# Kernel optimization log

Measured on AMD Instinct MI355X. Metric: run time of the kernel, lower is better.

## Reference

```python
import jax, jax.numpy as jnp
import numpy as np

B, S, H, E = 2, 2048, 16, 64
INV_SCALE = 8.0  # sqrt(head_dim); forward divides scores by this


def setup_inputs() -> dict:
    key = jax.random.key(0)
    ks = jax.random.split(key, 10)
    return {
        "query": jax.random.normal(ks[0], (B, S, H, E), dtype=jnp.float32),
        "key": jax.random.normal(ks[1], (B, S, H, E), dtype=jnp.float32),
        "value": jax.random.normal(ks[2], (B, S, H, E), dtype=jnp.float32),
        "attn_mask": jax.random.randint(ks[3], (B, S), 0, 2, dtype=jnp.int32),
        "Wq": jax.random.normal(ks[4], (E, E), dtype=jnp.float32) / np.sqrt(E),
        "bq": jax.random.normal(ks[5], (E,), dtype=jnp.float32) * 0.02,
        "Wk": jax.random.normal(ks[6], (E, E), dtype=jnp.float32) / np.sqrt(E),
        "bk": jax.random.normal(ks[7], (E,), dtype=jnp.float32) * 0.02,
        "Wv": jax.random.normal(ks[8], (E, E), dtype=jnp.float32) / np.sqrt(E),
        "bv": jax.random.normal(ks[9], (E,), dtype=jnp.float32) * 0.02,
    }


def reference(query, key, value, attn_mask, Wq, bq, Wk, bk, Wv, bv):
    # Linear projections over the last (embed) dim; torch Linear: x @ W.T + b
    q = jnp.einsum('bshe,fe->bhsf', query, Wq) + bq  # [B,H,S,E] (permute 0,2,1,3 fused)
    k = jnp.einsum('bshe,fe->bhsf', key, Wk) + bk
    v = jnp.einsum('bshe,fe->bhsf', value, Wv) + bv
    scores = jnp.einsum('bhqe,bhke->bhqk', q, k) / INV_SCALE  # [B,H,S,S]
    # mask: positions where attn_mask == 0 get -inf, broadcast over (1,1,k_len)
    masked = attn_mask[:, None, None, :] == 0  # [B,1,1,S]
    scores = jnp.where(masked, -jnp.inf, scores)
    attn = jax.nn.softmax(scores, axis=-1)
    out = jnp.einsum('bhqk,bhke->bqhe', attn, v)  # permute back to [B,S,H,E]
    return out
```

## Files before the change

kernel.cpp:

```cpp
#include <hip/hip_runtime.h>


#define BATCH 2
#define SEQ   2048
#define NH    16
#define DE    64
#define LDP   72
#define LDOF  68
#define NKT   (SEQ / 64)
#define LOG2E 1.44269504088896340736f
#define CSHIFT 16.0f

using bf16x8   = __attribute__((ext_vector_type(8))) __bf16;
using bf16x4   = __attribute__((ext_vector_type(4))) __bf16;
using floatx4  = __attribute__((ext_vector_type(4))) float;
using ushortx4 = __attribute__((ext_vector_type(4))) unsigned short;
using ushortx8 = __attribute__((ext_vector_type(8))) unsigned short;

__device__ __forceinline__ ushortx4 cvt4(floatx4 f) {
    bf16x4 h = __builtin_convertvector(f, bf16x4);
    return __builtin_bit_cast(ushortx4, h);
}

__device__ __forceinline__ void glds16(const unsigned short* g, unsigned short* l) {
    __builtin_amdgcn_global_load_lds(
        (const __attribute__((address_space(1))) unsigned int*)g,
        (__attribute__((address_space(3))) unsigned int*)l, 16, 0, 0);
}

__global__ __launch_bounds__(256) void proj_kernel(
    const float* __restrict__ xq, const float* __restrict__ xk, const float* __restrict__ xv,
    const float* __restrict__ Wq, const float* __restrict__ bq,
    const float* __restrict__ Wk, const float* __restrict__ bk,
    const float* __restrict__ Wv, const float* __restrict__ bv,
    unsigned short* __restrict__ qb, unsigned short* __restrict__ kb,
    unsigned short* __restrict__ vtb)
{
    __shared__ __align__(16) unsigned short Xb[64 * LDP];
    __shared__ __align__(16) unsigned short Wb[64 * LDP];
    __shared__ __align__(16) unsigned short Ob[64 * LDP];
    __shared__ float blds[64];

    const int t  = threadIdx.x;
    const int p  = blockIdx.x >> 10;
    const int bh = (blockIdx.x >> 5) & 31;
    const int st = blockIdx.x & 31;
    const int s0 = st * 64;
    const int b  = bh >> 4, h = bh & 15;
    const int lane = t & 63, w = t >> 6, quad = lane >> 4, l16 = lane & 15;

    const float* x    = (p == 0) ? xq : (p == 1) ? xk : xv;
    const float* W    = (p == 0) ? Wq : (p == 1) ? Wk : Wv;
    const float* bias = (p == 0) ? bq : (p == 1) ? bk : bv;

    #pragma unroll
    for (int i = 0; i < 4; ++i) {
        int idx = i * 1024 + t * 4;
        int row = idx >> 6, col = idx & 63;
        floatx4 xv4 = *(const floatx4*)(x + (((size_t)(b * SEQ + s0 + row) * NH + h) * DE + col));
        *(ushortx4*)&Xb[row * LDP + col] = cvt4(xv4);
        floatx4 wv4 = *(const floatx4*)(W + row * 64 + col);
        *(ushortx4*)&Wb[row * LDP + col] = cvt4(wv4);
    }
    if (t < 64) blds[t] = bias[t];
    __syncthreads();

    if (p < 2) {
        bf16x8 a0 = *(const bf16x8*)&Wb[(w * 16 + l16) * LDP + quad * 8];
        bf16x8 a1 = *(const bf16x8*)&Wb[(w * 16 + l16) * LDP + 32 + quad * 8];
        floatx4 bf4 = *(const floatx4*)&blds[w * 16 + quad * 4];
        const float scale = (p == 0) ? 0.125f * LOG2E : 1.0f;
        #pragma unroll
        for (int nb = 0; nb < 4; ++nb) {
            bf16x8 b0 = *(const bf16x8*)&Xb[(nb * 16 + l16) * LDP + quad * 8];
            bf16x8 b1 = *(const bf16x8*)&Xb[(nb * 16 + l16) * LDP + 32 + quad * 8];
            floatx4 c = {0.f, 0.f, 0.f, 0.f};
            c = __builtin_amdgcn_mfma_f32_16x16x32_bf16(a0, b0, c, 0, 0, 0);
            c = __builtin_amdgcn_mfma_f32_16x16x32_bf16(a1, b1, c, 0, 0, 0);
            floatx4 v;
            v[0] = (c[0] + bf4[0]) * scale; v[1] = (c[1] + bf4[1]) * scale;
            v[2] = (c[2] + bf4[2]) * scale; v[3] = (c[3] + bf4[3]) * scale;
            *(ushortx4*)&Ob[(nb * 16 + l16) * LDP + w * 16 + quad * 4] = cvt4(v);
        }
    } else {
        bf16x8 a0 = *(const bf16x8*)&Xb[(w * 16 + l16) * LDP + quad * 8];
        bf16x8 a1 = *(const bf16x8*)&Xb[(w * 16 + l16) * LDP + 32 + quad * 8];
        #pragma unroll
        for (int nb = 0; nb < 4; ++nb) {
            bf16x8 b0 = *(const bf16x8*)&Wb[(nb * 16 + l16) * LDP + quad * 8];
            bf16x8 b1 = *(const bf16x8*)&Wb[(nb * 16 + l16) * LDP + 32 + quad * 8];
            floatx4 c = {0.f, 0.f, 0.f, 0.f};
            c = __builtin_amdgcn_mfma_f32_16x16x32_bf16(a0, b0, c, 0, 0, 0);
            c = __builtin_amdgcn_mfma_f32_16x16x32_bf16(a1, b1, c, 0, 0, 0);
            float bw = blds[nb * 16 + l16];
            floatx4 v;
            v[0] = c[0] + bw; v[1] = c[1] + bw; v[2] = c[2] + bw; v[3] = c[3] + bw;
            *(ushortx4*)&Ob[(nb * 16 + l16) * LDP + w * 16 + quad * 4] = cvt4(v);
        }
    }
    __syncthreads();

    #pragma unroll
    for (int j = 0; j < 2; ++j) {
        int idx = j * 256 + t;
        int row = idx >> 3, c = idx & 7;
        int cp  = (c ^ (row & 7)) * 8;
        ushortx8 v = *(const ushortx8*)&Ob[row * LDP + c * 8];
        if (p < 2) {
            unsigned short* dst = (p == 0) ? qb : kb;
            *(ushortx8*)(dst + ((size_t)bh * SEQ + s0 + row) * DE + cp) = v;
        } else {
            *(ushortx8*)(vtb + ((size_t)bh * DE + row) * SEQ + s0 + cp) = v;
        }
    }
}

__global__ __launch_bounds__(512) void attn_kernel(
    const unsigned short* __restrict__ qb, const unsigned short* __restrict__ kb,
    const unsigned short* __restrict__ vtb, const int* __restrict__ mask,
    float* __restrict__ out)
{
    __shared__ __align__(16) char smem[16384 + 16384 + 18432 + 512];
    unsigned short* Kl = (unsigned short*)smem;
    unsigned short* Vl = (unsigned short*)(smem + 16384);
    unsigned short* Pq = (unsigned short*)(smem + 32768);
    float*          Ml = (float*)(smem + 32768 + 18432);
    float*          Ol = (float*)smem;

    const int t  = threadIdx.x;
    const int qt = blockIdx.x, bh = blockIdx.y;
    const int b  = bh >> 4, h = bh & 15;
    const int q0 = qt * 128;
    const int lane = t & 63, w = t >> 6;
    const int quad = lane >> 4, l16 = lane & 15;
    const int cS = ((quad ^ (l16 & 7)) * 8);

    const unsigned short* kbase = kb + (size_t)bh * SEQ * DE;
    const unsigned short* vbase = vtb + (size_t)bh * DE * SEQ;
    const unsigned short* qsrc  = qb + ((size_t)bh * SEQ + q0) * DE;
    const int* mrow = mask + b * SEQ;

    glds16(qsrc + (w * 16) * DE + lane * 8,      Pq + (w * 16) * 64);
    glds16(qsrc + (w * 16 + 8) * DE + lane * 8,  Pq + (w * 16 + 8) * 64);
    glds16(kbase + (size_t)(w * 8) * DE + lane * 8, Kl + w * 512);
    glds16(vbase + (size_t)(w * 8 + (lane >> 3)) * SEQ + (lane & 7) * 8, Vl + w * 512);
    if (t < 64) Ml[t] = mrow[t] ? 0.f : -1e30f;
    int mreg = (t < 64) ? mrow[64 + t] : 0;
    __syncthreads();

    bf16x8 qf0 = *(const bf16x8*)&Pq[(w * 16 + l16) * 64 + cS];
    bf16x8 qf1 = *(const bf16x8*)&Pq[(w * 16 + l16) * 64 + (cS ^ 32)];

    bf16x8 onesf;
    #pragma unroll
    for (int i = 0; i < 8; ++i) onesf[i] = (__bf16)1.0f;

    floatx4 o[4], acc_l;
    #pragma unroll
    for (int nb = 0; nb < 4; ++nb) o[nb] = floatx4{0.f, 0.f, 0.f, 0.f};
    acc_l = floatx4{0.f, 0.f, 0.f, 0.f};

    for (int kt = 0; kt < NKT; ++kt) {
        const int cur = kt & 1, nxt = cur ^ 1;
        const unsigned short* Kc = Kl + cur * 4096;
        const unsigned short* Vc = Vl + cur * 4096;
        const float*          Mc = Ml + cur * 64;

        if (kt + 1 < NKT) {
            const int k1 = (kt + 1) * 64;
            glds16(kbase + (size_t)(k1 + w * 8) * DE + lane * 8, Kl + nxt * 4096 + w * 512);
            glds16(vbase + (size_t)(w * 8 + (lane >> 3)) * SEQ + k1 + (lane & 7) * 8,
                   Vl + nxt * 4096 + w * 512);
            if (t < 64) Ml[nxt * 64 + t] = mreg ? 0.f : -1e30f;
            mreg = (t < 64 && kt + 2 < NKT) ? mrow[(kt + 2) * 64 + t] : 0;
        }

        floatx4 sc[4];
        #pragma unroll
        for (int sub = 0; sub < 4; ++sub) {
            const int r = sub * 16 + l16;
            bf16x8 kf0 = *(const bf16x8*)&Kc[r * 64 + cS];
            bf16x8 kf1 = *(const bf16x8*)&Kc[r * 64 + (cS ^ 32)];
            floatx4 c = *(const floatx4*)&Mc[sub * 16 + quad * 4];
            c = __builtin_amdgcn_mfma_f32_16x16x32_bf16(kf0, qf0, c, 0, 0, 0);
            c = __builtin_amdgcn_mfma_f32_16x16x32_bf16(kf1, qf1, c, 0, 0, 0);
            sc[sub] = c;
        }

        #pragma unroll
        for (int sub = 0; sub < 4; ++sub) {
            #pragma unroll
            for (int r = 0; r < 4; ++r)
                sc[sub][r] = __builtin_amdgcn_exp2f(sc[sub][r] - CSHIFT);
            *(ushortx4*)&Pq[(w * 16 + l16) * LDP + sub * 16 + quad * 4] = cvt4(sc[sub]);
        }
        __asm__ volatile("s_waitcnt lgkmcnt(0)" ::: "memory");

        bf16x8 pf0 = *(const bf16x8*)&Pq[(w * 16 + l16) * LDP + quad * 8];
        bf16x8 pf1 = *(const bf16x8*)&Pq[(w * 16 + l16) * LDP + 32 + quad * 8];
        #pragma unroll
        for (int nb = 0; nb < 4; ++nb) {
            const int r = nb * 16 + l16;
            bf16x8 vf0 = *(const bf16x8*)&Vc[r * 64 + cS];
            bf16x8 vf1 = *(const bf16x8*)&Vc[r * 64 + (cS ^ 32)];
            o[nb] = __builtin_amdgcn_mfma_f32_16x16x32_bf16(vf0, pf0, o[nb], 0, 0, 0);
            o[nb] = __builtin_amdgcn_mfma_f32_16x16x32_bf16(vf1, pf1, o[nb], 0, 0, 0);
        }
        acc_l = __builtin_amdgcn_mfma_f32_16x16x32_bf16(onesf, pf0, acc_l, 0, 0, 0);
        acc_l = __builtin_amdgcn_mfma_f32_16x16x32_bf16(onesf, pf1, acc_l, 0, 0, 0);

        __syncthreads();
    }

    float invl = __builtin_amdgcn_rcpf(acc_l[0]);
    #pragma unroll
    for (int nb = 0; nb < 4; ++nb) {
        floatx4 ov;
        ov[0] = o[nb][0] * invl; ov[1] = o[nb][1] * invl;
        ov[2] = o[nb][2] * invl; ov[3] = o[nb][3] * invl;
        *(floatx4*)&Ol[(w * 16 + l16) * LDOF + nb * 16 + quad * 4] = ov;
    }
    __asm__ volatile("s_waitcnt lgkmcnt(0)" ::: "memory");
    #pragma unroll
    for (int pass = 0; pass < 4; ++pass) {
        int rl  = w * 16 + pass * 4 + quad;
        int col = l16 * 4;
        floatx4 tv = *(const floatx4*)&Ol[rl * LDOF + col];
        *(floatx4*)(out + (((size_t)b * SEQ + q0 + rl) * NH + h) * DE + col) = tv;
    }
}

extern "C" void kernel_launch(void* const* d_in, const int* in_sizes, int n_in,
                              void* d_out, int out_size, void* d_ws, size_t ws_size,
                              hipStream_t stream) {
    const float* query = (const float*)d_in[0];
    const float* key   = (const float*)d_in[1];
    const float* value = (const float*)d_in[2];
    const int*   mask  = (const int*)d_in[3];
    const float* Wq = (const float*)d_in[4];
    const float* bq = (const float*)d_in[5];
    const float* Wk = (const float*)d_in[6];
    const float* bk = (const float*)d_in[7];
    const float* Wv = (const float*)d_in[8];
    const float* bv = (const float*)d_in[9];

    const size_t tensor_elems = (size_t)BATCH * NH * SEQ * DE;
    unsigned short* qb  = (unsigned short*)d_ws;
    unsigned short* kb  = qb + tensor_elems;
    unsigned short* vtb = kb + tensor_elems;

    proj_kernel<<<dim3(3 * BATCH * NH * (SEQ / 64)), 256, 0, stream>>>(
        query, key, value, Wq, bq, Wk, bk, Wv, bv, qb, kb, vtb);
    attn_kernel<<<dim3(SEQ / 128, BATCH * NH), 512, 0, stream>>>(
        qb, kb, vtb, mask, (float*)d_out);
}
```

Baseline: 158.5 us.

## Switch attention to 32x32x16 MFMA with in-register P via permlane32 swap

Restructures the attention inner loop to use 32x32x16 bf16 MFMAs. Each wave now owns 32 query rows and half of the 64-key block, and the per-tile split results are combined through LDS at the end. The softmax probabilities are packed to bf16 and rearranged in registers with v_permlane32_swap instead of a round trip through LDS. The row sum is accumulated with scalar adds rather than extra ones-MFMAs, and the exp shift is folded into the mask bias. In exchange it adds a cross-wave reduction epilogue with extra syncs, and sets launch bounds to request 4 blocks per SM.

```diff
diff --git a/kernel.cpp b/kernel.cpp
--- a/kernel.cpp
+++ b/kernel.cpp
@@ -13,13 +13,26 @@
 
 using bf16x8   = __attribute__((ext_vector_type(8))) __bf16;
 using bf16x4   = __attribute__((ext_vector_type(4))) __bf16;
+using bf16x2   = __attribute__((ext_vector_type(2))) __bf16;
+using floatx2  = __attribute__((ext_vector_type(2))) float;
 using floatx4  = __attribute__((ext_vector_type(4))) float;
+using floatx16 = __attribute__((ext_vector_type(16))) float;
 using ushortx4 = __attribute__((ext_vector_type(4))) unsigned short;
 using ushortx8 = __attribute__((ext_vector_type(8))) unsigned short;
+using uintx4   = __attribute__((ext_vector_type(4))) unsigned int;
 
 __device__ __forceinline__ ushortx4 cvt4(floatx4 f) {
     bf16x4 h = __builtin_convertvector(f, bf16x4);
     return __builtin_bit_cast(ushortx4, h);
+}
+
+__device__ __forceinline__ unsigned int pkbf16(float a, float b) {
+    floatx2 f = {a, b};
+    return __builtin_bit_cast(unsigned int, __builtin_convertvector(f, bf16x2));
+}
+
+__device__ __forceinline__ void pl32swap(unsigned int& x, unsigned int& y) {
+    __asm__ volatile("v_permlane32_swap_b32 %0, %1" : "+v"(x), "+v"(y));
 }
 
 __device__ __forceinline__ void glds16(const unsigned short* g, unsigned short* l) {
@@ -115,25 +128,27 @@
     }
 }
 
-__global__ __launch_bounds__(512) void attn_kernel(
+__global__ __launch_bounds__(512, 4) void attn_kernel(
     const unsigned short* __restrict__ qb, const unsigned short* __restrict__ kb,
     const unsigned short* __restrict__ vtb, const int* __restrict__ mask,
     float* __restrict__ out)
 {
-    __shared__ __align__(16) char smem[16384 + 16384 + 18432 + 512];
+    __shared__ __align__(16) char smem[16384 + 16384 + 16384 + 512];
     unsigned short* Kl = (unsigned short*)smem;
     unsigned short* Vl = (unsigned short*)(smem + 16384);
     unsigned short* Pq = (unsigned short*)(smem + 32768);
-    float*          Ml = (float*)(smem + 32768 + 18432);
+    float*          Ml = (float*)(smem + 49152);
     float*          Ol = (float*)smem;
+    float*          Ll = (float*)(smem + 34816);
 
     const int t  = threadIdx.x;
     const int qt = blockIdx.x, bh = blockIdx.y;
     const int b  = bh >> 4, h = bh & 15;
     const int q0 = qt * 128;
     const int lane = t & 63, w = t >> 6;
-    const int quad = lane >> 4, l16 = lane & 15;
-    const int cS = ((quad ^ (l16 & 7)) * 8);
+    const int hi = lane >> 5, l31 = lane & 31;
+    const int qw = w & 3, kblk = w >> 2;
+    const int sw7 = l31 & 7;
 
     const unsigned short* kbase = kb + (size_t)bh * SEQ * DE;
     const unsigned short* vbase = vtb + (size_t)bh * DE * SEQ;
@@ -144,21 +159,19 @@
     glds16(qsrc + (w * 16 + 8) * DE + lane * 8,  Pq + (w * 16 + 8) * 64);
     glds16(kbase + (size_t)(w * 8) * DE + lane * 8, Kl + w * 512);
     glds16(vbase + (size_t)(w * 8 + (lane >> 3)) * SEQ + (lane & 7) * 8, Vl + w * 512);
-    if (t < 64) Ml[t] = mrow[t] ? 0.f : -1e30f;
+    if (t < 64) Ml[t] = mrow[t] ? -CSHIFT : -1e30f;
     int mreg = (t < 64) ? mrow[64 + t] : 0;
     __syncthreads();
 
-    bf16x8 qf0 = *(const bf16x8*)&Pq[(w * 16 + l16) * 64 + cS];
-    bf16x8 qf1 = *(const bf16x8*)&Pq[(w * 16 + l16) * 64 + (cS ^ 32)];
-
-    bf16x8 onesf;
+    bf16x8 qf[4];
     #pragma unroll
-    for (int i = 0; i < 8; ++i) onesf[i] = (__bf16)1.0f;
-
-    floatx4 o[4], acc_l;
+    for (int ks = 0; ks < 4; ++ks)
+        qf[ks] = *(const bf16x8*)&Pq[(qw * 32 + l31) * 64 + (((ks * 2 + hi) ^ sw7) * 8)];
+
+    floatx16 o0, o1;
     #pragma unroll
-    for (int nb = 0; nb < 4; ++nb) o[nb] = floatx4{0.f, 0.f, 0.f, 0.f};
-    acc_l = floatx4{0.f, 0.f, 0.f, 0.f};
+    for (int i = 0; i < 16; ++i) { o0[i] = 0.f; o1[i] = 0.f; }
+    float lp = 0.f;
 
     for (int kt = 0; kt < NKT; ++kt) {
         const int cur = kt & 1, nxt = cur ^ 1;
@@ -171,62 +184,95 @@
             glds16(kbase + (size_t)(k1 + w * 8) * DE + lane * 8, Kl + nxt * 4096 + w * 512);
             glds16(vbase + (size_t)(w * 8 + (lane >> 3)) * SEQ + k1 + (lane & 7) * 8,
                    Vl + nxt * 4096 + w * 512);
-            if (t < 64) Ml[nxt * 64 + t] = mreg ? 0.f : -1e30f;
+            if (t < 64) Ml[nxt * 64 + t] = mreg ? -CSHIFT : -1e30f;
             mreg = (t < 64 && kt + 2 < NKT) ? mrow[(kt + 2) * 64 + t] : 0;
         }
 
-        floatx4 sc[4];
-        #pragma unroll
-        for (int sub = 0; sub < 4; ++sub) {
-            const int r = sub * 16 + l16;
-            bf16x8 kf0 = *(const bf16x8*)&Kc[r * 64 + cS];
-            bf16x8 kf1 = *(const bf16x8*)&Kc[r * 64 + (cS ^ 32)];
-            floatx4 c = *(const floatx4*)&Mc[sub * 16 + quad * 4];
-            c = __builtin_amdgcn_mfma_f32_16x16x32_bf16(kf0, qf0, c, 0, 0, 0);
-            c = __builtin_amdgcn_mfma_f32_16x16x32_bf16(kf1, qf1, c, 0, 0, 0);
-            sc[sub] = c;
-        }
-
-        #pragma unroll
-        for (int sub = 0; sub < 4; ++sub) {
-            #pragma unroll
-            for (int r = 0; r < 4; ++r)
-                sc[sub][r] = __builtin_amdgcn_exp2f(sc[sub][r] - CSHIFT);
-            *(ushortx4*)&Pq[(w * 16 + l16) * LDP + sub * 16 + quad * 4] = cvt4(sc[sub]);
-        }
-        __asm__ volatile("s_waitcnt lgkmcnt(0)" ::: "memory");
-
-        bf16x8 pf0 = *(const bf16x8*)&Pq[(w * 16 + l16) * LDP + quad * 8];
-        bf16x8 pf1 = *(const bf16x8*)&Pq[(w * 16 + l16) * LDP + 32 + quad * 8];
-        #pragma unroll
-        for (int nb = 0; nb < 4; ++nb) {
-            const int r = nb * 16 + l16;
-            bf16x8 vf0 = *(const bf16x8*)&Vc[r * 64 + cS];
-            bf16x8 vf1 = *(const bf16x8*)&Vc[r * 64 + (cS ^ 32)];
-            o[nb] = __builtin_amdgcn_mfma_f32_16x16x32_bf16(vf0, pf0, o[nb], 0, 0, 0);
-            o[nb] = __builtin_amdgcn_mfma_f32_16x16x32_bf16(vf1, pf1, o[nb], 0, 0, 0);
-        }
-        acc_l = __builtin_amdgcn_mfma_f32_16x16x32_bf16(onesf, pf0, acc_l, 0, 0, 0);
-        acc_l = __builtin_amdgcn_mfma_f32_16x16x32_bf16(onesf, pf1, acc_l, 0, 0, 0);
+        floatx16 sc;
+        #pragma unroll
+        for (int g = 0; g < 4; ++g) {
+            floatx4 mb = *(const floatx4*)&Mc[kblk * 32 + g * 8 + hi * 4];
+            sc[4 * g + 0] = mb[0]; sc[4 * g + 1] = mb[1];
+            sc[4 * g + 2] = mb[2]; sc[4 * g + 3] = mb[3];
+        }
+        #pragma unroll
+        for (int ks = 0; ks < 4; ++ks) {
+            bf16x8 kf = *(const bf16x8*)&Kc[(kblk * 32 + l31) * 64 + (((ks * 2 + hi) ^ sw7) * 8)];
+            sc = __builtin_amdgcn_mfma_f32_32x32x16_bf16(kf, qf[ks], sc, 0, 0, 0);
+        }
+
+        #pragma unroll
+        for (int r = 0; r < 16; ++r)
+            sc[r] = __builtin_amdgcn_exp2f(sc[r]);
+        {
+            float a0 = sc[0] + sc[1],   a1 = sc[2] + sc[3];
+            float a2 = sc[4] + sc[5],   a3 = sc[6] + sc[7];
+            float a4 = sc[8] + sc[9],   a5 = sc[10] + sc[11];
+            float a6 = sc[12] + sc[13], a7 = sc[14] + sc[15];
+            lp += ((a0 + a1) + (a2 + a3)) + ((a4 + a5) + (a6 + a7));
+        }
+
+        unsigned int wd0 = pkbf16(sc[0], sc[1]),   wd1 = pkbf16(sc[2], sc[3]);
+        unsigned int wd2 = pkbf16(sc[4], sc[5]),   wd3 = pkbf16(sc[6], sc[7]);
+        unsigned int wd4 = pkbf16(sc[8], sc[9]),   wd5 = pkbf16(sc[10], sc[11]);
+        unsigned int wd6 = pkbf16(sc[12], sc[13]), wd7 = pkbf16(sc[14], sc[15]);
+        pl32swap(wd0, wd2); pl32swap(wd1, wd3);
+        pl32swap(wd4, wd6); pl32swap(wd5, wd7);
+        uintx4 f0v = {wd0, wd1, wd2, wd3};
+        uintx4 f1v = {wd4, wd5, wd6, wd7};
+        bf16x8 pf0 = __builtin_bit_cast(bf16x8, f0v);
+        bf16x8 pf1 = __builtin_bit_cast(bf16x8, f1v);
+
+        #pragma unroll
+        for (int s = 0; s < 2; ++s) {
+            const bf16x8 pf = s ? pf1 : pf0;
+            const int cc = ((kblk * 4 + s * 2 + hi) ^ sw7) * 8;
+            bf16x8 v0 = *(const bf16x8*)&Vc[l31 * 64 + cc];
+            bf16x8 v1 = *(const bf16x8*)&Vc[(32 + l31) * 64 + cc];
+            o0 = __builtin_amdgcn_mfma_f32_32x32x16_bf16(v0, pf, o0, 0, 0, 0);
+            o1 = __builtin_amdgcn_mfma_f32_32x32x16_bf16(v1, pf, o1, 0, 0, 0);
+        }
 
         __syncthreads();
     }
 
-    float invl = __builtin_amdgcn_rcpf(acc_l[0]);
-    #pragma unroll
-    for (int nb = 0; nb < 4; ++nb) {
-        floatx4 ov;
-        ov[0] = o[nb][0] * invl; ov[1] = o[nb][1] * invl;
-        ov[2] = o[nb][2] * invl; ov[3] = o[nb][3] * invl;
-        *(floatx4*)&Ol[(w * 16 + l16) * LDOF + nb * 16 + quad * 4] = ov;
-    }
-    __asm__ volatile("s_waitcnt lgkmcnt(0)" ::: "memory");
-    #pragma unroll
-    for (int pass = 0; pass < 4; ++pass) {
-        int rl  = w * 16 + pass * 4 + quad;
-        int col = l16 * 4;
-        floatx4 tv = *(const floatx4*)&Ol[rl * LDOF + col];
-        *(floatx4*)(out + (((size_t)b * SEQ + q0 + rl) * NH + h) * DE + col) = tv;
+    const int qrow = qw * 32 + l31;
+    Ll[qrow * 4 + kblk * 2 + hi] = lp;
+    if (kblk == 1) {
+        #pragma unroll
+        for (int g = 0; g < 4; ++g) {
+            floatx4 t0 = {o0[4*g+0], o0[4*g+1], o0[4*g+2], o0[4*g+3]};
+            *(floatx4*)&Ol[qrow * LDOF + g * 8 + hi * 4] = t0;
+            floatx4 t1 = {o1[4*g+0], o1[4*g+1], o1[4*g+2], o1[4*g+3]};
+            *(floatx4*)&Ol[qrow * LDOF + 32 + g * 8 + hi * 4] = t1;
+        }
+    }
+    __syncthreads();
+    if (kblk == 0) {
+        floatx4 lv = *(const floatx4*)&Ll[qrow * 4];
+        float invl = __builtin_amdgcn_rcpf(lv[0] + lv[1] + lv[2] + lv[3]);
+        #pragma unroll
+        for (int g = 0; g < 4; ++g) {
+            floatx4 t0 = *(floatx4*)&Ol[qrow * LDOF + g * 8 + hi * 4];
+            t0[0] = (t0[0] + o0[4*g+0]) * invl; t0[1] = (t0[1] + o0[4*g+1]) * invl;
+            t0[2] = (t0[2] + o0[4*g+2]) * invl; t0[3] = (t0[3] + o0[4*g+3]) * invl;
+            *(floatx4*)&Ol[qrow * LDOF + g * 8 + hi * 4] = t0;
+            floatx4 t1 = *(floatx4*)&Ol[qrow * LDOF + 32 + g * 8 + hi * 4];
+            t1[0] = (t1[0] + o1[4*g+0]) * invl; t1[1] = (t1[1] + o1[4*g+1]) * invl;
+            t1[2] = (t1[2] + o1[4*g+2]) * invl; t1[3] = (t1[3] + o1[4*g+3]) * invl;
+            *(floatx4*)&Ol[qrow * LDOF + 32 + g * 8 + hi * 4] = t1;
+        }
+    }
+    __syncthreads();
+    {
+        const int quad = lane >> 4, l16 = lane & 15;
+        #pragma unroll
+        for (int pass = 0; pass < 4; ++pass) {
+            int rl  = w * 16 + pass * 4 + quad;
+            int col = l16 * 4;
+            floatx4 tv = *(const floatx4*)&Ol[rl * LDOF + col];
+            *(floatx4*)(out + (((size_t)b * SEQ + q0 + rl) * NH + h) * DE + col) = tv;
+        }
     }
 }
 
```

Result: faster. 150.9 us (-4.8%).
